# Kernel optimization log

Hardware: AMD Instinct MI355X
Metric: run time of the kernel (lower is better)

Reference implementation:

```python
import jax, jax.numpy as jnp
import numpy as np

NATOMS_PER_TYPE = (128, 128)  # natom = 256 split across 2 atom types
EI_MEAN = (-3.37, -4.50)
NFEAT, H1, H2 = 42, 50, 50


def _fcnet(x, W0, b0, W1, b1, W2, b2):
    # x: [B, n_type, F]; tanh MLP, linear output head -> per-atom energy [B, n_type, 1]
    h0 = jnp.tanh(x @ W0 + b0)
    h1 = jnp.tanh(h0 @ W1 + b1)
    return h1 @ W2 + b2


def _ei_all(image, params):
    # per-atom-type MLP over contiguous atom slices, concat -> Ei [B, natom, 1]
    outs, off = [], 0
    for t, n in enumerate(NATOMS_PER_TYPE):
        outs.append(_fcnet(image[:, off:off + n], *params[t]))
        off += n
    return jnp.concatenate(outs, axis=1)


def setup_inputs() -> dict:
    key = jax.random.key(0)
    ks = jax.random.split(key, 16)
    B, natom, nn = 32, 256, 100
    inp = {
        'image': jax.random.normal(ks[0], (B, natom, NFEAT), dtype=jnp.float32),
        'dfeat': jax.random.normal(ks[1], (B, natom, nn, NFEAT, 3), dtype=jnp.float32),
        'neighbor': jax.random.randint(ks[2], (B, natom, nn), 0, natom + 1, dtype=jnp.int64),
    }
    def xav(k, fan_in, fan_out):
        s = np.sqrt(6.0 / (fan_in + fan_out))
        return jax.random.uniform(k, (fan_in, fan_out), jnp.float32, -s, s)
    for t in range(2):
        kk = jax.random.split(ks[3 + t], 3)
        inp[f'W0_t{t}'] = xav(kk[0], NFEAT, H1)
        inp[f'b0_t{t}'] = jnp.zeros((H1,), jnp.float32)
        inp[f'W1_t{t}'] = xav(kk[1], H1, H2)
        inp[f'b1_t{t}'] = jnp.zeros((H2,), jnp.float32)
        inp[f'W2_t{t}'] = xav(kk[2], H2, 1)
        inp[f'b2_t{t}'] = jnp.array([EI_MEAN[t]], jnp.float32)
    return inp


def reference(image, dfeat, neighbor,
              W0_t0, b0_t0, W1_t0, b1_t0, W2_t0, b2_t0,
              W0_t1, b0_t1, W1_t1, b1_t1, W2_t1, b2_t1):
    params = ((W0_t0, b0_t0, W1_t0, b1_t0, W2_t0, b2_t0),
              (W0_t1, b0_t1, W1_t1, b1_t1, W2_t1, b2_t1))
    Ei = _ei_all(image, params)          # [B, natom, 1]
    Etot = Ei.sum(axis=1)                # [B, 1]
    # test_grad = d(sum Ei)/d(image), matches torch.autograd.grad in the original
    test_grad = jax.grad(lambda img: _ei_all(img, params).sum())(image)  # [B, natom, F]
    B, natom, F = image.shape
    # fortran-style: index 0 -> zero row (no neighbor), 1..natom -> atoms
    dE_pad = jnp.concatenate([jnp.zeros((B, 1, F), image.dtype), test_grad], axis=1)
    nbr_dE = dE_pad[jnp.arange(B)[:, None, None], neighbor]  # [B, natom, nn, F]
    Force = jnp.einsum('bnkf,bnkfd->bnd', nbr_dE, dfeat)     # [B, natom, 3]
    return (Etot, Ei, Force)
```

## Files before the change

kernel.cpp:

```cpp
#include <hip/hip_runtime.h>
#include <cstdint>

#define BB 32
#define NATOM 256
#define NN 100
#define NF 42
#define HH 50
#define PADROWS 257
#define DE_STRIDE (PADROWS * NF)

__global__ __launch_bounds__(128) void mlp_fwd_bwd(
    const float* __restrict__ image,
    const float* __restrict__ W0a, const float* __restrict__ b0a,
    const float* __restrict__ W1a, const float* __restrict__ b1a,
    const float* __restrict__ W2a, const float* __restrict__ b2a,
    const float* __restrict__ W0b, const float* __restrict__ b0b,
    const float* __restrict__ W1b, const float* __restrict__ b1b,
    const float* __restrict__ W2b, const float* __restrict__ b2b,
    float* __restrict__ outEtot,
    float* __restrict__ outEi,
    float* __restrict__ dEp)
{
    __shared__ float W0s[NF * HH];
    __shared__ float W1s[HH * HH];
    __shared__ float W2s[HH], b0s[HH], b1s[HH];
    __shared__ float b2s;
    __shared__ float red[128];

    const int blk  = blockIdx.x;
    const int b    = blk >> 1;
    const int half = blk & 1;
    const int tid  = threadIdx.x;

    const float* W0 = half ? W0b : W0a;
    const float* b0 = half ? b0b : b0a;
    const float* W1 = half ? W1b : W1a;
    const float* b1 = half ? b1b : b1a;
    const float* W2 = half ? W2b : W2a;
    const float* b2 = half ? b2b : b2a;

    for (int i = tid; i < NF * HH; i += 128) W0s[i] = W0[i];
    for (int i = tid; i < HH * HH; i += 128) W1s[i] = W1[i];
    if (tid < HH) { W2s[tid] = W2[tid]; b0s[tid] = b0[tid]; b1s[tid] = b1[tid]; }
    if (tid == 0) b2s = b2[0];

    if (half == 0 && tid < NF) dEp[(size_t)b * DE_STRIDE + tid] = 0.0f;
    __syncthreads();

    const int n = half * 128 + tid;
    const int g = b * NATOM + n;

    float x[NF];
    {
        const float* xp = image + (size_t)g * NF;
        #pragma unroll
        for (int f = 0; f < NF; ++f) x[f] = xp[f];
    }

    float h0[HH], h1[HH];

    for (int j = 0; j < HH; j += 2) {
        float s0 = b0s[j], s1 = b0s[j + 1];
        #pragma unroll
        for (int f = 0; f < NF; ++f) {
            const float xf = x[f];
            s0 += xf * W0s[f * HH + j];
            s1 += xf * W0s[f * HH + j + 1];
        }
        h0[j] = tanhf(s0);
        h0[j + 1] = tanhf(s1);
    }

    for (int j = 0; j < HH; j += 2) {
        float s0 = b1s[j], s1 = b1s[j + 1];
        #pragma unroll
        for (int i = 0; i < HH; ++i) {
            const float hi = h0[i];
            s0 += hi * W1s[i * HH + j];
            s1 += hi * W1s[i * HH + j + 1];
        }
        h1[j] = tanhf(s0);
        h1[j + 1] = tanhf(s1);
    }

    float Ei0 = 0.0f, Ei1 = 0.0f;
    for (int j = 0; j < HH; j += 2) {
        Ei0 += h1[j] * W2s[j];
        Ei1 += h1[j + 1] * W2s[j + 1];
    }
    const float Ei = Ei0 + Ei1 + b2s;
    outEi[g] = Ei;

    red[tid] = Ei;
    __syncthreads();
    for (int o = 64; o > 0; o >>= 1) {
        if (tid < o) red[tid] += red[tid + o];
        __syncthreads();
    }
    if (tid == 0) atomicAdd(&outEtot[b], red[0]);

    #pragma unroll
    for (int j = 0; j < HH; ++j) {
        const float t = h1[j];
        h1[j] = W2s[j] * (1.0f - t * t);
    }
    for (int i = 0; i < HH; i += 2) {
        float s0 = 0.0f, s1 = 0.0f;
        #pragma unroll
        for (int j = 0; j < HH; ++j) {
            const float gj = h1[j];
            s0 += gj * W1s[i * HH + j];
            s1 += gj * W1s[(i + 1) * HH + j];
        }
        const float t0 = h0[i], t1 = h0[i + 1];
        h0[i] = s0 * (1.0f - t0 * t0);
        h0[i + 1] = s1 * (1.0f - t1 * t1);
    }
    float* dxp = dEp + (size_t)b * DE_STRIDE + (size_t)(1 + n) * NF;
    for (int f = 0; f < NF; f += 2) {
        float s0 = 0.0f, s1 = 0.0f;
        #pragma unroll
        for (int i = 0; i < HH; ++i) {
            const float gi = h0[i];
            s0 += gi * W0s[f * HH + i];
            s1 += gi * W0s[(f + 1) * HH + i];
        }
        dxp[f] = s0;
        dxp[f + 1] = s1;
    }
}

__global__ __launch_bounds__(256) void force_kernel(
    const float* __restrict__ dfeat,
    const int* __restrict__ neighbor,
    const float* __restrict__ dEp,
    float* __restrict__ outForce)
{
    __shared__ int   nbr_s[NN];
    __shared__ float dE_s[NN * NF];
    __shared__ float red[3 * 256];

    const int bn  = blockIdx.x;
    const int b   = bn >> 8;
    const int tid = threadIdx.x;

    if (tid < NN) nbr_s[tid] = neighbor[(size_t)bn * NN + tid];
    __syncthreads();

    {
        const float* dEb = dEp + (size_t)b * DE_STRIDE;
        for (int q = tid; q < NN * NF; q += 256) {
            const int k = q / NF;
            const int f = q - k * NF;
            dE_s[q] = dEb[nbr_s[k] * NF + f];
        }
    }
    __syncthreads();

    const int w = tid >> 6;
    const int l = tid & 63;

    int off0 = 0, off1 = 0, off2 = 0, off3 = 0;
    int d0 = 0, d1 = 0, d2 = 0, d3 = 0;
    float acc0 = 0.0f, acc1 = 0.0f, acc2 = 0.0f, acc3 = 0.0f;
    const bool active = (l < 63);
    if (active) {
        const int r = 4 * l;
        #define DECOMP(c, OFF, DD) { int rc = r + (c); int ko = (rc >= 126) ? 1 : 0; \
            int rr = rc - 126 * ko; int f = rr / 3; (DD) = rr - 3 * f; (OFF) = ko * NF + f; }
        DECOMP(0, off0, d0) DECOMP(1, off1, d1) DECOMP(2, off2, d2) DECOMP(3, off3, d3)
        #undef DECOMP

        const float4* df4 = (const float4*)dfeat + (size_t)bn * 3150;
        for (int p = w; p < 50; p += 4) {
            const float4 v = df4[p * 63 + l];
            const float* base = dE_s + 84 * p;
            acc0 += v.x * base[off0];
            acc1 += v.y * base[off1];
            acc2 += v.z * base[off2];
            acc3 += v.w * base[off3];
        }
    }

    const float s0 = (d0 == 0 ? acc0 : 0.0f) + (d1 == 0 ? acc1 : 0.0f) +
                     (d2 == 0 ? acc2 : 0.0f) + (d3 == 0 ? acc3 : 0.0f);
    const float s1 = (d0 == 1 ? acc0 : 0.0f) + (d1 == 1 ? acc1 : 0.0f) +
                     (d2 == 1 ? acc2 : 0.0f) + (d3 == 1 ? acc3 : 0.0f);
    const float s2 = (d0 == 2 ? acc0 : 0.0f) + (d1 == 2 ? acc1 : 0.0f) +
                     (d2 == 2 ? acc2 : 0.0f) + (d3 == 2 ? acc3 : 0.0f);

    red[tid] = s0; red[256 + tid] = s1; red[512 + tid] = s2;
    __syncthreads();
    for (int o = 128; o > 0; o >>= 1) {
        if (tid < o) {
            red[tid]       += red[tid + o];
            red[256 + tid] += red[256 + tid + o];
            red[512 + tid] += red[512 + tid + o];
        }
        __syncthreads();
    }
    if (tid < 3) outForce[(size_t)bn * 3 + tid] = red[tid * 256];
}

extern "C" void kernel_launch(void* const* d_in, const int* in_sizes, int n_in,
                              void* d_out, int out_size, void* d_ws, size_t ws_size,
                              hipStream_t stream) {
    const float* image    = (const float*)d_in[0];
    const float* dfeat    = (const float*)d_in[1];
    const int*   neighbor = (const int*)d_in[2];
    const float* W0_t0 = (const float*)d_in[3];
    const float* b0_t0 = (const float*)d_in[4];
    const float* W1_t0 = (const float*)d_in[5];
    const float* b1_t0 = (const float*)d_in[6];
    const float* W2_t0 = (const float*)d_in[7];
    const float* b2_t0 = (const float*)d_in[8];
    const float* W0_t1 = (const float*)d_in[9];
    const float* b0_t1 = (const float*)d_in[10];
    const float* W1_t1 = (const float*)d_in[11];
    const float* b1_t1 = (const float*)d_in[12];
    const float* W2_t1 = (const float*)d_in[13];
    const float* b2_t1 = (const float*)d_in[14];

    float* outEtot  = (float*)d_out;
    float* outEi    = outEtot + BB;
    float* outForce = outEi + BB * NATOM;
    float* dEp      = (float*)d_ws;

    hipMemsetAsync(d_out, 0, BB * sizeof(float), stream);

    mlp_fwd_bwd<<<64, 128, 0, stream>>>(
        image,
        W0_t0, b0_t0, W1_t0, b1_t0, W2_t0, b2_t0,
        W0_t1, b0_t1, W1_t1, b1_t1, W2_t1, b2_t1,
        outEtot, outEi, dEp);

    force_kernel<<<BB * NATOM, 256, 0, stream>>>(dfeat, neighbor, dEp, outForce);
}
```

Measured before the change: 637.5 us.

## Prefetch dfeat before gather, use wavefront-shuffle reduction, fast tanh, vectorized IO

In the force kernel, each wave now issues all of its dfeat float4 loads into registers before the neighbor gather into shared memory, so the large HBM stream overlaps with the gather and barrier. The 768-entry shared-memory tree reduction is replaced by wave-level xor shuffles plus a 4-entry combine. The MLP kernel swaps tanhf for an exp-based approximation and uses float2 loads and stores. The register-held prefetch adds VGPR pressure, and the fast tanh trades a little accuracy.

```diff
diff --git a/kernel.cpp b/kernel.cpp
--- a/kernel.cpp
+++ b/kernel.cpp
@@ -8,6 +8,11 @@
 #define HH 50
 #define PADROWS 257
 #define DE_STRIDE (PADROWS * NF)
+
+__device__ __forceinline__ float fast_tanh(float x) {
+    const float e = __expf(2.0f * x);
+    return 1.0f - 2.0f / (e + 1.0f);
+}
 
 __global__ __launch_bounds__(128) void mlp_fwd_bwd(
     const float* __restrict__ image,
@@ -52,9 +57,13 @@
 
     float x[NF];
     {
-        const float* xp = image + (size_t)g * NF;
-        #pragma unroll
-        for (int f = 0; f < NF; ++f) x[f] = xp[f];
+        const float2* xp = (const float2*)(image + (size_t)g * NF);
+        #pragma unroll
+        for (int f = 0; f < NF / 2; ++f) {
+            const float2 v = xp[f];
+            x[2 * f] = v.x;
+            x[2 * f + 1] = v.y;
+        }
     }
 
     float h0[HH], h1[HH];
@@ -67,8 +76,8 @@
             s0 += xf * W0s[f * HH + j];
             s1 += xf * W0s[f * HH + j + 1];
         }
-        h0[j] = tanhf(s0);
-        h0[j + 1] = tanhf(s1);
+        h0[j] = fast_tanh(s0);
+        h0[j + 1] = fast_tanh(s1);
     }
 
     for (int j = 0; j < HH; j += 2) {
@@ -79,8 +88,8 @@
             s0 += hi * W1s[i * HH + j];
             s1 += hi * W1s[i * HH + j + 1];
         }
-        h1[j] = tanhf(s0);
-        h1[j + 1] = tanhf(s1);
+        h1[j] = fast_tanh(s0);
+        h1[j + 1] = fast_tanh(s1);
     }
 
     float Ei0 = 0.0f, Ei1 = 0.0f;
@@ -116,7 +125,7 @@
         h0[i] = s0 * (1.0f - t0 * t0);
         h0[i + 1] = s1 * (1.0f - t1 * t1);
     }
-    float* dxp = dEp + (size_t)b * DE_STRIDE + (size_t)(1 + n) * NF;
+    float2* dxp = (float2*)(dEp + (size_t)b * DE_STRIDE + (size_t)(1 + n) * NF);
     for (int f = 0; f < NF; f += 2) {
         float s0 = 0.0f, s1 = 0.0f;
         #pragma unroll
@@ -125,8 +134,7 @@
             s0 += gi * W0s[f * HH + i];
             s1 += gi * W0s[(f + 1) * HH + i];
         }
-        dxp[f] = s0;
-        dxp[f + 1] = s1;
+        dxp[f >> 1] = make_float2(s0, s1);
     }
 }
 
@@ -138,15 +146,31 @@
 {
     __shared__ int   nbr_s[NN];
     __shared__ float dE_s[NN * NF];
-    __shared__ float red[3 * 256];
+    __shared__ float part[4][3];
 
     const int bn  = blockIdx.x;
     const int b   = bn >> 8;
     const int tid = threadIdx.x;
+    const int w   = tid >> 6;
+    const int l   = tid & 63;
+
+    const int start = (w < 2) ? 13 * w : 26 + 12 * (w - 2);
+    const int cnt   = (w < 2) ? 13 : 12;
+
+    float4 v[13];
+    const float4* df4 = (const float4*)dfeat + (size_t)bn * 3150;
+    if (l < 63) {
+        #pragma unroll
+        for (int i = 0; i < 13; ++i) {
+            int p = start + i;
+            if (p > 49) p = 49;
+            v[i] = df4[p * 63 + l];
+        }
+        if (w >= 2) v[12] = make_float4(0.0f, 0.0f, 0.0f, 0.0f);
+    }
 
     if (tid < NN) nbr_s[tid] = neighbor[(size_t)bn * NN + tid];
     __syncthreads();
-
     {
         const float* dEb = dEp + (size_t)b * DE_STRIDE;
         for (int q = tid; q < NN * NF; q += 256) {
@@ -157,49 +181,47 @@
     }
     __syncthreads();
 
-    const int w = tid >> 6;
-    const int l = tid & 63;
-
-    int off0 = 0, off1 = 0, off2 = 0, off3 = 0;
+    float acc0 = 0.0f, acc1 = 0.0f, acc2 = 0.0f, acc3 = 0.0f;
     int d0 = 0, d1 = 0, d2 = 0, d3 = 0;
-    float acc0 = 0.0f, acc1 = 0.0f, acc2 = 0.0f, acc3 = 0.0f;
-    const bool active = (l < 63);
-    if (active) {
+    float s0 = 0.0f, s1 = 0.0f, s2 = 0.0f;
+    if (l < 63) {
+        int off0, off1, off2, off3;
         const int r = 4 * l;
         #define DECOMP(c, OFF, DD) { int rc = r + (c); int ko = (rc >= 126) ? 1 : 0; \
             int rr = rc - 126 * ko; int f = rr / 3; (DD) = rr - 3 * f; (OFF) = ko * NF + f; }
         DECOMP(0, off0, d0) DECOMP(1, off1, d1) DECOMP(2, off2, d2) DECOMP(3, off3, d3)
         #undef DECOMP
 
-        const float4* df4 = (const float4*)dfeat + (size_t)bn * 3150;
-        for (int p = w; p < 50; p += 4) {
-            const float4 v = df4[p * 63 + l];
+        #pragma unroll
+        for (int i = 0; i < 13; ++i) {
+            int p = start + i;
+            if (p > 49) p = 49;
             const float* base = dE_s + 84 * p;
-            acc0 += v.x * base[off0];
-            acc1 += v.y * base[off1];
-            acc2 += v.z * base[off2];
-            acc3 += v.w * base[off3];
-        }
-    }
-
-    const float s0 = (d0 == 0 ? acc0 : 0.0f) + (d1 == 0 ? acc1 : 0.0f) +
-                     (d2 == 0 ? acc2 : 0.0f) + (d3 == 0 ? acc3 : 0.0f);
-    const float s1 = (d0 == 1 ? acc0 : 0.0f) + (d1 == 1 ? acc1 : 0.0f) +
-                     (d2 == 1 ? acc2 : 0.0f) + (d3 == 1 ? acc3 : 0.0f);
-    const float s2 = (d0 == 2 ? acc0 : 0.0f) + (d1 == 2 ? acc1 : 0.0f) +
-                     (d2 == 2 ? acc2 : 0.0f) + (d3 == 2 ? acc3 : 0.0f);
-
-    red[tid] = s0; red[256 + tid] = s1; red[512 + tid] = s2;
-    __syncthreads();
-    for (int o = 128; o > 0; o >>= 1) {
-        if (tid < o) {
-            red[tid]       += red[tid + o];
-            red[256 + tid] += red[256 + tid + o];
-            red[512 + tid] += red[512 + tid + o];
-        }
-        __syncthreads();
-    }
-    if (tid < 3) outForce[(size_t)bn * 3 + tid] = red[tid * 256];
+            acc0 += v[i].x * base[off0];
+            acc1 += v[i].y * base[off1];
+            acc2 += v[i].z * base[off2];
+            acc3 += v[i].w * base[off3];
+        }
+
+        s0 = (d0 == 0 ? acc0 : 0.0f) + (d1 == 0 ? acc1 : 0.0f) +
+             (d2 == 0 ? acc2 : 0.0f) + (d3 == 0 ? acc3 : 0.0f);
+        s1 = (d0 == 1 ? acc0 : 0.0f) + (d1 == 1 ? acc1 : 0.0f) +
+             (d2 == 1 ? acc2 : 0.0f) + (d3 == 1 ? acc3 : 0.0f);
+        s2 = (d0 == 2 ? acc0 : 0.0f) + (d1 == 2 ? acc1 : 0.0f) +
+             (d2 == 2 ? acc2 : 0.0f) + (d3 == 2 ? acc3 : 0.0f);
+    }
+
+    #pragma unroll
+    for (int m = 32; m > 0; m >>= 1) {
+        s0 += __shfl_xor(s0, m);
+        s1 += __shfl_xor(s1, m);
+        s2 += __shfl_xor(s2, m);
+    }
+    if (l == 0) { part[w][0] = s0; part[w][1] = s1; part[w][2] = s2; }
+    __syncthreads();
+    if (tid < 3)
+        outForce[(size_t)bn * 3 + tid] =
+            part[0][tid] + part[1][tid] + part[2][tid] + part[3][tid];
 }
 
 extern "C" void kernel_launch(void* const* d_in, const int* in_sizes, int n_in,
```

Result: no change. 625.4 us (-1.9%).
